# Kernel optimization log

Hardware: AMD Instinct MI355X
Metric: run time of the kernel (lower is better)

Reference implementation:

```python
import jax, jax.numpy as jnp
import numpy as np
from jax import lax

BASE = 10000.0
N_STATE = 4096
N_HEAD = 32
H_DIM = N_STATE // N_HEAD          # 128
NUM_ROT = H_DIM // 2               # 64
BATCH, SEQ = 4, 2048


def setup_inputs() -> dict:
    key = jax.random.key(0)
    k1, k2, k3, k4 = jax.random.split(key, 4)
    x = jax.random.normal(k1, (BATCH, SEQ, N_STATE), dtype=jnp.float32)
    thetas = jax.random.normal(k2, (NUM_ROT,), dtype=jnp.float32) * 0.1
    rotation_pairs = jax.random.uniform(k3, (NUM_ROT, 2), dtype=jnp.float32) * H_DIM
    theta_scale = jnp.ones((1,), dtype=jnp.float32)
    rotation_matrix = jnp.eye(H_DIM, dtype=jnp.float32) + 0.02 * jax.random.normal(k4, (H_DIM, H_DIM), dtype=jnp.float32)
    inv_freq = (1.0 / BASE ** (jnp.arange(0, H_DIM, 2, dtype=jnp.float32) / H_DIM)).astype(jnp.float32)
    return {"x": x, "thetas": thetas, "rotation_pairs": rotation_pairs,
            "theta_scale": theta_scale, "rotation_matrix": rotation_matrix,
            "inv_freq": inv_freq, "n_head": N_HEAD}


def _apply(x, thetas, rotation_pairs, theta_scale, rotation_matrix, inv_freq, n_head):
    B, S, n_state = x.shape
    h_dim = rotation_matrix.shape[0]
    xf = x.reshape(B, S, n_head, h_dim).reshape(-1, h_dim)  # [B*S*H, h_dim]

    idx = rotation_pairs.astype(jnp.int32)          # [R,2] Givens pair indices
    th = thetas * theta_scale[0]                    # [R]

    def body(xc, inp):
        i, j, t = inp
        c, s = jnp.cos(t), jnp.sin(t)
        xi = xc[:, i]
        xj = xc[:, j]
        same = (i == j)
        # x @ G touches only columns i and j (matches torch G construction,
        # including the i==j overwrite case where G[i,i] ends as cos)
        vi = jnp.where(same, xi * c, xi * c + xj * s)
        vj = jnp.where(same, xi * c, -xi * s + xj * c)
        xc = xc.at[:, i].set(vi)
        xc = xc.at[:, j].set(vj)
        return xc, None

    xf, _ = lax.scan(body, xf, (idx[:, 0], idx[:, 1], th))
    xf = xf @ rotation_matrix                       # learned h_dim x h_dim mix
    xh = xf.reshape(B, S, n_head, h_dim)

    pos = jnp.arange(S, dtype=jnp.float32)
    sinusoid = pos[:, None] * inv_freq[None, :]     # [S, h_dim/2]
    sin = jnp.sin(sinusoid)[None, :, None, :]
    cos = jnp.cos(sinusoid)[None, :, None, :]
    x1 = xh[..., ::2]
    x2 = xh[..., 1::2]
    out = jnp.concatenate([x1 * cos - x2 * sin, x1 * sin + x2 * cos], axis=-1)
    return out.reshape(B, S, n_state)


def reference(x, thetas, rotation_pairs, theta_scale, rotation_matrix, inv_freq, n_head):
    return _apply(x, thetas, rotation_pairs, theta_scale, rotation_matrix, inv_freq, n_head)
```

## Files before the change

kernel.cpp:

```cpp
#include <hip/hip_runtime.h>
#include <hip/hip_bf16.h>
#include <math.h>

#define SEQ_LEN 2048
#define NROWS (4 * 2048 * 32)
#define NSTRIPS (NROWS / 16)

typedef short bf16x8 __attribute__((ext_vector_type(8)));
typedef float f32x4 __attribute__((ext_vector_type(4)));

__device__ __forceinline__ unsigned short f2bf(float f) {
    union { float f; unsigned int i; } v; v.f = f;
    unsigned int r = v.i + 0x7FFFu + ((v.i >> 16) & 1u);
    return (unsigned short)(r >> 16);
}

__global__ void prep_kernel(const float* __restrict__ thetas,
                            const float* __restrict__ pairs,
                            const float* __restrict__ tscale,
                            const float* __restrict__ rotmat,
                            unsigned short* __restrict__ Bsw) {
    __shared__ float M[128][128];
    __shared__ float Cv[64], Sv[64];
    __shared__ int   Iv[64], Jv[64];
    const int t = threadIdx.x;
    if (t < 64) {
        const float th = thetas[t] * tscale[0];
        Cv[t] = cosf(th);
        Sv[t] = sinf(th);
        int i = (int)pairs[2 * t];
        int j = (int)pairs[2 * t + 1];
        Iv[t] = min(max(i, 0), 127);
        Jv[t] = min(max(j, 0), 127);
    }
    float* Mf = &M[0][0];
#pragma unroll 8
    for (int idx = t; idx < 128 * 128; idx += 256) Mf[idx] = rotmat[idx];
    __syncthreads();
    if (t < 128) {
        for (int r = 63; r >= 0; --r) {
            const int i = Iv[r], j = Jv[r];
            const float c = Cv[r], s = Sv[r];
            if (i == j) {
                M[i][t] *= c;
            } else {
                const float a = M[i][t], b = M[j][t];
                M[i][t] = c * a - s * b;
                M[j][t] = s * a + c * b;
            }
        }
    }
    __syncthreads();
    for (int idx = t; idx < 32 * 64; idx += 256) {
        const int f = idx >> 6, lane = idx & 63;
        const int kk = f >> 3, nt = f & 7;
        const int krow = kk * 32 + (lane >> 4) * 8;
        const int m = lane & 15;
        const int col = (nt < 4) ? (8 * m + 2 * nt) : (8 * m + 2 * (nt - 4) + 1);
        unsigned short* dst = Bsw + (size_t)idx * 8;
#pragma unroll
        for (int j2 = 0; j2 < 8; ++j2) dst[j2] = f2bf(M[krow + j2][col]);
    }
}

__global__ __launch_bounds__(256, 4) void rope_kernel(
        const float* __restrict__ x,
        const unsigned short* __restrict__ Bsw,
        const float* __restrict__ invfreq,
        float* __restrict__ out) {
    __shared__ f32x4 Blds[2048];
    const int tid = threadIdx.x;
    const int lane = tid & 63;
    const int w = tid >> 6;
    {
        const char* gbase = (const char*)Bsw;
#pragma unroll
        for (int i = 0; i < 8; ++i) {
            const int fi = i * 256 + w * 64;
            __builtin_amdgcn_global_load_lds(
                (const __attribute__((address_space(1))) unsigned int*)
                    (gbase + (size_t)(fi + lane) * 16),
                (__attribute__((address_space(3))) unsigned int*)&Blds[fi],
                16, 0, 0);
        }
    }

    const int wave = (int)(blockIdx.x * 4 + w);
    const int m = lane & 15;
    const int quad = lane >> 4;
    const int sA = wave;
    const int sB = wave + 8192;

    const float* xA = x + (size_t)(sA * 16 + m) * 128 + quad * 8;
    const float* xB = x + (size_t)(sB * 16 + m) * 128 + quad * 8;
    f32x4 loA[4], hiA[4], loB[4], hiB[4];
#pragma unroll
    for (int kk = 0; kk < 4; ++kk) {
        loA[kk] = *(const f32x4*)(xA + kk * 32);
        hiA[kk] = *(const f32x4*)(xA + kk * 32 + 4);
    }
#pragma unroll
    for (int kk = 0; kk < 4; ++kk) {
        loB[kk] = *(const f32x4*)(xB + kk * 32);
        hiB[kk] = *(const f32x4*)(xB + kk * 32 + 4);
    }

    const float invf = invfreq[lane];
    float snA, csA, snB, csB;
    sincosf((float)((sA * 16 >> 5) & (SEQ_LEN - 1)) * invf, &snA, &csA);
    sincosf((float)((sB * 16 >> 5) & (SEQ_LEN - 1)) * invf, &snB, &csB);

    __syncthreads();

    const bf16x8* Bf = (const bf16x8*)Blds;

#pragma unroll
    for (int half = 0; half < 2; ++half) {
        const int r0 = (half ? sB : sA) * 16;
        const f32x4* lo = half ? loB : loA;
        const f32x4* hi = half ? hiB : hiA;
        const float sn_l = half ? snB : snA;
        const float cs_l = half ? csB : csA;

        bf16x8 A[4];
#pragma unroll
        for (int kk = 0; kk < 4; ++kk) {
            union { __hip_bfloat162 h; unsigned int u; } c0, c1, c2, c3;
            c0.h = __float22bfloat162_rn(make_float2(lo[kk][0], lo[kk][1]));
            c1.h = __float22bfloat162_rn(make_float2(lo[kk][2], lo[kk][3]));
            c2.h = __float22bfloat162_rn(make_float2(hi[kk][0], hi[kk][1]));
            c3.h = __float22bfloat162_rn(make_float2(hi[kk][2], hi[kk][3]));
            union { unsigned int u[4]; bf16x8 v; } a;
            a.u[0] = c0.u; a.u[1] = c1.u; a.u[2] = c2.u; a.u[3] = c3.u;
            A[kk] = a.v;
        }

        f32x4 acc[8];
#pragma unroll
        for (int nt = 0; nt < 8; ++nt) acc[nt] = (f32x4){0.f, 0.f, 0.f, 0.f};

#pragma unroll
        for (int kk = 0; kk < 4; ++kk)
#pragma unroll
            for (int nt = 0; nt < 8; ++nt)
                acc[nt] = __builtin_amdgcn_mfma_f32_16x16x32_bf16(
                    A[kk], Bf[(kk * 8 + nt) * 64 + lane], acc[nt], 0, 0, 0);

        float cs[4], sn[4];
#pragma unroll
        for (int nt = 0; nt < 4; ++nt) {
            cs[nt] = __shfl(cs_l, 4 * m + nt, 64);
            sn[nt] = __shfl(sn_l, 4 * m + nt, 64);
        }
        float* orow = out + (size_t)(r0 + quad * 4) * 128;
#pragma unroll
        for (int rr = 0; rr < 4; ++rr) {
            f32x4 ve, vo;
#pragma unroll
            for (int nt = 0; nt < 4; ++nt) {
                const float ye = acc[nt][rr];
                const float yo = acc[nt + 4][rr];
                ve[nt] = ye * cs[nt] - yo * sn[nt];
                vo[nt] = ye * sn[nt] + yo * cs[nt];
            }
            *(f32x4*)(orow + (size_t)rr * 128 + 4 * m)      = ve;
            *(f32x4*)(orow + (size_t)rr * 128 + 64 + 4 * m) = vo;
        }
    }
}

extern "C" void kernel_launch(void* const* d_in, const int* in_sizes, int n_in,
                              void* d_out, int out_size, void* d_ws, size_t ws_size,
                              hipStream_t stream) {
    const float* x      = (const float*)d_in[0];
    const float* thetas = (const float*)d_in[1];
    const float* pairs  = (const float*)d_in[2];
    const float* tscale = (const float*)d_in[3];
    const float* rotmat = (const float*)d_in[4];
    const float* invfr  = (const float*)d_in[5];
    float* out = (float*)d_out;
    unsigned short* Bsw = (unsigned short*)d_ws;

    prep_kernel<<<1, 256, 0, stream>>>(thetas, pairs, tscale, rotmat, Bsw);
    rope_kernel<<<2048, 256, 0, stream>>>(x, Bsw, invfr, out);
}
```

Before: 263.0 us.

## Process four strips per wave with double-buffered register prefetch

Result: no change. 261.3 us (-0.6%).

```diff
diff --git a/kernel.cpp b/kernel.cpp
--- a/kernel.cpp
+++ b/kernel.cpp
@@ -88,39 +88,30 @@
     const int wave = (int)(blockIdx.x * 4 + w);
     const int m = lane & 15;
     const int quad = lane >> 4;
-    const int sA = wave;
-    const int sB = wave + 8192;
+    const bf16x8* Bf = (const bf16x8*)Blds;
+    const float invf = invfreq[lane];
 
-    const float* xA = x + (size_t)(sA * 16 + m) * 128 + quad * 8;
-    const float* xB = x + (size_t)(sB * 16 + m) * 128 + quad * 8;
-    f32x4 loA[4], hiA[4], loB[4], hiB[4];
+    const int s0 = wave;
+    const int s1 = wave + 4096;
+    const int s2 = wave + 8192;
+    const int s3 = wave + 12288;
+
+    f32x4 lo0[4], hi0[4], lo1[4], hi1[4];
+
+    auto PREFETCH = [&](f32x4* lo, f32x4* hi, int s) {
+        const float* xs = x + (size_t)(s * 16 + m) * 128 + quad * 8;
 #pragma unroll
-    for (int kk = 0; kk < 4; ++kk) {
-        loA[kk] = *(const f32x4*)(xA + kk * 32);
-        hiA[kk] = *(const f32x4*)(xA + kk * 32 + 4);
-    }
-#pragma unroll
-    for (int kk = 0; kk < 4; ++kk) {
-        loB[kk] = *(const f32x4*)(xB + kk * 32);
-        hiB[kk] = *(const f32x4*)(xB + kk * 32 + 4);
-    }
+        for (int kk = 0; kk < 4; ++kk) {
+            lo[kk] = *(const f32x4*)(xs + kk * 32);
+            hi[kk] = *(const f32x4*)(xs + kk * 32 + 4);
+        }
+    };
 
-    const float invf = invfreq[lane];
-    float snA, csA, snB, csB;
-    sincosf((float)((sA * 16 >> 5) & (SEQ_LEN - 1)) * invf, &snA, &csA);
-    sincosf((float)((sB * 16 >> 5) & (SEQ_LEN - 1)) * invf, &snB, &csB);
-
-    __syncthreads();
-
-    const bf16x8* Bf = (const bf16x8*)Blds;
-
-#pragma unroll
-    for (int half = 0; half < 2; ++half) {
-        const int r0 = (half ? sB : sA) * 16;
-        const f32x4* lo = half ? loB : loA;
-        const f32x4* hi = half ? hiB : hiA;
-        const float sn_l = half ? snB : snA;
-        const float cs_l = half ? csB : csA;
+    auto COMPUTE = [&](const f32x4* lo, const f32x4* hi, int s) {
+        const int r0 = s * 16;
+        const int s_pos = (s >> 1) & (SEQ_LEN - 1);
+        float sn_l, cs_l;
+        sincosf((float)s_pos * invf, &sn_l, &cs_l);
 
         bf16x8 A[4];
 #pragma unroll
@@ -166,7 +157,24 @@
             *(f32x4*)(orow + (size_t)rr * 128 + 4 * m)      = ve;
             *(f32x4*)(orow + (size_t)rr * 128 + 64 + 4 * m) = vo;
         }
-    }
+    };
+
+    PREFETCH(lo0, hi0, s0);
+    __syncthreads();
+
+    PREFETCH(lo1, hi1, s1);
+    __builtin_amdgcn_sched_barrier(0);
+    COMPUTE(lo0, hi0, s0);
+
+    PREFETCH(lo0, hi0, s2);
+    __builtin_amdgcn_sched_barrier(0);
+    COMPUTE(lo1, hi1, s1);
+
+    PREFETCH(lo1, hi1, s3);
+    __builtin_amdgcn_sched_barrier(0);
+    COMPUTE(lo0, hi0, s2);
+
+    COMPUTE(lo1, hi1, s3);
 }
 
 extern "C" void kernel_launch(void* const* d_in, const int* in_sizes, int n_in,
@@ -182,5 +190,5 @@
     unsigned short* Bsw = (unsigned short*)d_ws;
 
     prep_kernel<<<1, 256, 0, stream>>>(thetas, pairs, tscale, rotmat, Bsw);
-    rope_kernel<<<2048, 256, 0, stream>>>(x, Bsw, invfr, out);
+    rope_kernel<<<1024, 256, 0, stream>>>(x, Bsw, invfr, out);
 }
```
